# Optimization experiments

Hardware: AMD Instinct MI355X
Metric: run time of the kernel (lower is better)

The kernel has to match this reference:

```python
import jax, jax.numpy as jnp
import numpy as np

NUM_FEATS = 65536
IN_SIZE = 1024
OUT_SIZE = 1024
NUM_MODULES = 8


def setup_inputs() -> dict:
    key = jax.random.key(0)
    k1, k2, k3, k4 = jax.random.split(key, 4)
    in_feats = jax.random.normal(k1, (NUM_FEATS, IN_SIZE), dtype=jnp.float32)
    module_ids = jax.random.randint(k2, (NUM_FEATS,), 0, NUM_MODULES, dtype=jnp.int64)
    # Per-expert Linear parameters (same architecture, different weights).
    # PyTorch nn.Linear default init: U(-1/sqrt(in), 1/sqrt(in)).
    bound = 1.0 / np.sqrt(IN_SIZE)
    W = jax.random.uniform(k3, (NUM_MODULES, IN_SIZE, OUT_SIZE), jnp.float32, -bound, bound)
    b = jax.random.uniform(k4, (NUM_MODULES, OUT_SIZE), jnp.float32, -bound, bound)
    return {"in_feats": in_feats, "module_ids": module_ids, "W": W, "b": b}


def reference(in_feats, module_ids, W, b):
    # Faithful to: out[mask_e] = Linear_e(in_feats[mask_e]) for each expert e.
    # Vectorized as a fixed small loop over experts with masked combine
    # (no Python loop over the data dimension).
    num_feats = in_feats.shape[0]
    out = jnp.zeros((num_feats, OUT_SIZE), dtype=in_feats.dtype)
    for e in range(NUM_MODULES):
        y = in_feats @ W[e] + b[e]  # [num_feats, OUT_SIZE]
        mask = (module_ids == e)[:, None]
        out = jnp.where(mask, y, out)
    return out
```

## Files before the change

kernel.cpp:

```cpp
#include <hip/hip_runtime.h>

typedef unsigned short u16;
typedef unsigned int u32;
typedef __attribute__((ext_vector_type(8))) short short8;
typedef __attribute__((ext_vector_type(4))) float f32x4;

#define NF 65536
#define KDIM 1024
#define NDIM 1024
#define NE 8
#define BM 128
#define BN 128
#define MAX_MT (NF / BM + NE)
#define GEMM_GRID (MAX_MT * 8)
#define TILE_B 16384
#define SORT_BLOCKS 64

#define AS1 __attribute__((address_space(1)))
#define AS3 __attribute__((address_space(3)))

__device__ __forceinline__ u16 f2bf(float f) {
  u32 u = __float_as_uint(f);
  u += 0x7FFF + ((u >> 16) & 1);
  return (u16)(u >> 16);
}

__device__ __forceinline__ int swz8(int r) {
  return (r & 7) ^ ((r >> 3) & 7);
}
__device__ __forceinline__ int swz_slot(int r) { return swz8(r) << 4; }

__device__ __forceinline__ void cp16(void* l, const void* g) {
  __builtin_amdgcn_global_load_lds((const AS1 unsigned int*)g,
                                   (AS3 unsigned int*)l, 16, 0, 0);
}

__global__ void k_cnt(const int* __restrict__ ids, int* __restrict__ gcnt) {
  __shared__ int wc[16][NE];
  int b = blockIdx.x, t = threadIdx.x;
  int w = t >> 6, lane = t & 63;
  if (t < 16 * NE) ((int*)wc)[t] = 0;
  __syncthreads();
  for (int s = 0; s < 4; ++s) {
    int i = (b << 10) + (s << 8) + t;
    int e = ids[i];
#pragma unroll
    for (int ee = 0; ee < NE; ++ee) {
      unsigned long long mask = __ballot(e == ee);
      if (lane == 0) wc[(s << 2) + w][ee] = (int)__popcll(mask);
    }
  }
  __syncthreads();
  if (t < NE) {
    int sum = 0;
#pragma unroll
    for (int j = 0; j < 16; ++j) sum += wc[j][t];
    gcnt[b * NE + t] = sum;
  }
}

__global__ void k_excl(const int* __restrict__ gcnt, int* __restrict__ counts,
                       int* __restrict__ offsets, int* __restrict__ tile_base,
                       int* __restrict__ base) {
  __shared__ int tot[NE], offs[NE];
  int t = threadIdx.x;
  if (t < NE) {
    int s = 0;
    for (int b = 0; b < SORT_BLOCKS; ++b) s += gcnt[b * NE + t];
    tot[t] = s;
    counts[t] = s;
  }
  __syncthreads();
  if (t == 0) {
    int run = 0, tb = 0;
    tile_base[0] = 0;
    for (int e = 0; e < NE; ++e) {
      offsets[e] = run;
      offs[e] = run;
      run += tot[e];
      tb += (tot[e] + BM - 1) / BM;
      tile_base[e + 1] = tb;
    }
  }
  __syncthreads();
  if (t < NE) {
    int run = offs[t];
    for (int b = 0; b < SORT_BLOCKS; ++b) {
      base[b * NE + t] = run;
      run += gcnt[b * NE + t];
    }
  }
}

__global__ void k_place(const int* __restrict__ ids, const int* __restrict__ base,
                        int* __restrict__ perm) {
  __shared__ int wc[16][NE], wsc[16][NE];
  int b = blockIdx.x, t = threadIdx.x;
  int w = t >> 6, lane = t & 63;
  for (int s = 0; s < 4; ++s) {
    int i = (b << 10) + (s << 8) + t;
    int e = ids[i];
#pragma unroll
    for (int ee = 0; ee < NE; ++ee) {
      unsigned long long mask = __ballot(e == ee);
      if (lane == 0) wc[(s << 2) + w][ee] = (int)__popcll(mask);
    }
  }
  __syncthreads();
  if (t < NE) {
    int run = 0;
#pragma unroll
    for (int j = 0; j < 16; ++j) {
      wsc[j][t] = run;
      run += wc[j][t];
    }
  }
  __syncthreads();
  for (int s = 0; s < 4; ++s) {
    int i = (b << 10) + (s << 8) + t;
    int e = ids[i];
#pragma unroll
    for (int ee = 0; ee < NE; ++ee) {
      unsigned long long mask = __ballot(e == ee);
      if (e == ee) {
        int rank = (int)__popcll(mask & ((1ull << lane) - 1ull));
        perm[base[b * NE + e] + wsc[(s << 2) + w][e] + rank] = i;
      }
    }
  }
}

__global__ void k_aconv(const float* __restrict__ A, const int* __restrict__ perm,
                        const int* __restrict__ counts,
                        const int* __restrict__ offsets,
                        const int* __restrict__ tile_base, u16* __restrict__ Abf) {
  int b = blockIdx.x;
  int mt = b >> 4, kt = b & 15;
  if (mt >= tile_base[NE]) return;
  int e = 0;
#pragma unroll
  for (int ee = 0; ee < NE - 1; ++ee)
    if (mt >= tile_base[ee + 1]) e = ee + 1;
  int mloc = mt - tile_base[e];
  int row_base = offsets[e] + (mloc << 7);
  int rim = counts[e] - (mloc << 7);
  rim = rim < BM ? rim : BM;
  int tid = threadIdx.x;
  char* dst = (char*)Abf + (size_t)b * TILE_B;
#pragma unroll
  for (int i = 0; i < 4; ++i) {
    int o = (i << 12) + (tid << 4);
    int r = o >> 7;
    int s = ((o >> 4) & 7) ^ swz8(r);
    uint4 pkt = make_uint4(0, 0, 0, 0);
    if (r < rim) {
      int g = perm[row_base + r];
      const float* src = A + (size_t)g * KDIM + (kt << 6) + (s << 3);
      float4 v0 = ((const float4*)src)[0];
      float4 v1 = ((const float4*)src)[1];
      pkt.x = (u32)f2bf(v0.x) | ((u32)f2bf(v0.y) << 16);
      pkt.y = (u32)f2bf(v0.z) | ((u32)f2bf(v0.w) << 16);
      pkt.z = (u32)f2bf(v1.x) | ((u32)f2bf(v1.y) << 16);
      pkt.w = (u32)f2bf(v1.z) | ((u32)f2bf(v1.w) << 16);
    }
    *(uint4*)(dst + o) = pkt;
  }
}

__global__ void k_wconv2(const float* __restrict__ W, u16* __restrict__ Wt) {
  int b = blockIdx.x;
  int e = b >> 7, nt = (b >> 4) & 7, kt = b & 15;
  int tid = threadIdx.x;
  const float* We = W + ((size_t)e << 20);
  char* dst = (char*)Wt + (size_t)b * TILE_B;
#pragma unroll
  for (int i = 0; i < 4; ++i) {
    int o = (i << 12) + (tid << 4);
    int r = o >> 7;
    int s = ((o >> 4) & 7) ^ swz8(r);
    int n = (nt << 7) + r;
    int k = (kt << 6) + (s << 3);
    u32 p[4];
#pragma unroll
    for (int j = 0; j < 4; ++j) {
      u32 lo = f2bf(We[(size_t)(k + 2 * j) * NDIM + n]);
      u32 hi = f2bf(We[(size_t)(k + 2 * j + 1) * NDIM + n]);
      p[j] = lo | (hi << 16);
    }
    *(uint4*)(dst + o) = make_uint4(p[0], p[1], p[2], p[3]);
  }
}

__global__ __launch_bounds__(256, 4) void k_gemm_fast(
    const u16* __restrict__ Abf, const u16* __restrict__ Wt,
    const float* __restrict__ bias, const int* __restrict__ perm,
    const int* __restrict__ offsets, const int* __restrict__ counts,
    const int* __restrict__ tile_base, float* __restrict__ out) {
  int bid = blockIdx.x;
  const int cpx = GEMM_GRID >> 3;
  int l = (bid & 7) * cpx + (bid >> 3);
  int mt = l >> 3, nt = l & 7;
  if (mt >= tile_base[NE]) return;
  int e = 0;
#pragma unroll
  for (int ee = 0; ee < NE - 1; ++ee)
    if (mt >= tile_base[ee + 1]) e = ee + 1;
  int mloc = mt - tile_base[e];
  int row_base = offsets[e] + (mloc << 7);
  int rim = counts[e] - (mloc << 7);
  rim = rim < BM ? rim : BM;
  int n0 = nt << 7;

  __shared__ __align__(16) char lds[2 * TILE_B];
  char* la = lds;
  char* lb = lds + TILE_B;

  int tid = threadIdx.x;
  int lane = tid & 63, wid = tid >> 6;
  int wr = wid >> 1, wc = wid & 1;
  int l15 = lane & 15;
  int lk2 = (lane >> 4) << 4;

  const char* srcA = (const char*)Abf + (size_t)(mt << 4) * TILE_B;
  const char* srcB = (const char*)Wt + (size_t)(((e << 3) + nt) << 4) * TILE_B;

  int ar_addr[4], br_addr[4];
#pragma unroll
  for (int m = 0; m < 4; ++m) {
    int r = (wr << 6) + (m << 4) + l15;
    ar_addr[m] = r * 128 + (lk2 ^ swz_slot(r));
  }
#pragma unroll
  for (int n = 0; n < 4; ++n) {
    int r = (wc << 6) + (n << 4) + l15;
    br_addr[n] = r * 128 + (lk2 ^ swz_slot(r));
  }

  f32x4 acc[4][4];
#pragma unroll
  for (int m = 0; m < 4; ++m)
#pragma unroll
    for (int n = 0; n < 4; ++n) acc[m][n] = f32x4{0.f, 0.f, 0.f, 0.f};

  int toff = tid << 4;
#pragma unroll 1
  for (int kt = 0; kt < KDIM / 64; ++kt) {
    __syncthreads();
    const char* ga = srcA + kt * TILE_B;
    const char* gb = srcB + kt * TILE_B;
#pragma unroll
    for (int j = 0; j < 4; ++j) cp16(la + toff + (j << 12), ga + toff + (j << 12));
#pragma unroll
    for (int j = 0; j < 4; ++j) cp16(lb + toff + (j << 12), gb + toff + (j << 12));
    asm volatile("s_waitcnt vmcnt(0)" ::: "memory");
    __builtin_amdgcn_sched_barrier(0);
    __syncthreads();
#pragma unroll
    for (int kk = 0; kk < 2; ++kk) {
      int kx = kk << 6;
      short8 af[4], bfr[4];
#pragma unroll
      for (int m = 0; m < 4; ++m)
        af[m] = __builtin_bit_cast(short8, *(const uint4*)(la + (ar_addr[m] ^ kx)));
#pragma unroll
      for (int n = 0; n < 4; ++n)
        bfr[n] = __builtin_bit_cast(short8, *(const uint4*)(lb + (br_addr[n] ^ kx)));
#pragma unroll
      for (int m = 0; m < 4; ++m)
#pragma unroll
        for (int n = 0; n < 4; ++n)
          acc[m][n] = __builtin_amdgcn_mfma_f32_16x16x32_bf16(af[m], bfr[n],
                                                              acc[m][n], 0, 0, 0);
    }
  }

  float bv[4];
#pragma unroll
  for (int n = 0; n < 4; ++n)
    bv[n] = bias[(e << 10) + n0 + (wc << 6) + (n << 4) + l15];
  int rq = (lane >> 4) << 2;
#pragma unroll
  for (int m = 0; m < 4; ++m) {
#pragma unroll
    for (int j = 0; j < 4; ++j) {
      int rl = (wr << 6) + (m << 4) + rq + j;
      if (rl < rim) {
        int grow = perm[row_base + rl];
        float* orow = out + (size_t)grow * NDIM + n0 + (wc << 6) + l15;
#pragma unroll
        for (int n = 0; n < 4; ++n) orow[n << 4] = acc[m][n][j] + bv[n];
      }
    }
  }
}

__global__ __launch_bounds__(256, 3) void k_gemm_slow(
    const float* __restrict__ A, const float* __restrict__ W,
    const float* __restrict__ bias, const int* __restrict__ perm,
    const int* __restrict__ offsets, const int* __restrict__ counts,
    const int* __restrict__ tile_base, float* __restrict__ out) {
  int bid = blockIdx.x;
  const int cpx = GEMM_GRID >> 3;
  int l = (bid & 7) * cpx + (bid >> 3);
  int mt = l >> 3, nt = l & 7;
  if (mt >= tile_base[NE]) return;
  int e = 0;
#pragma unroll
  for (int ee = 0; ee < NE - 1; ++ee)
    if (mt >= tile_base[ee + 1]) e = ee + 1;
  int mloc = mt - tile_base[e];
  int row_base = offsets[e] + (mloc << 7);
  int rim = counts[e] - (mloc << 7);
  rim = rim < BM ? rim : BM;
  int n0 = nt << 7;

  __shared__ u16 Al[BM * 64];
  __shared__ u16 Bl[BN * 64];
  char* alb = (char*)Al;
  char* blb = (char*)Bl;

  int tid = threadIdx.x;
  int lane = tid & 63, wid = tid >> 6;
  int wr = wid >> 1, wc = wid & 1;
  int l15 = lane & 15;
  int lk2 = (lane >> 4) << 4;

  int acol4 = tid & 15, argp = tid >> 4;
  const float* arow_p[8];
  int aswz[8];
#pragma unroll
  for (int i = 0; i < 8; ++i) {
    int r = argp + (i << 4);
    int rr = r < rim ? r : rim - 1;
    int grow = perm[row_base + rr];
    arow_p[i] = A + (size_t)grow * KDIM + (acol4 << 2);
    aswz[i] = r * 128 + ((acol4 << 3) ^ swz_slot(r));
  }
  int bnloc = tid & 127;
  int bkh = tid >> 7;
  const float* bcol_f = W + ((size_t)e << 20) + n0 + bnloc;
  int bswz[4];
#pragma unroll
  for (int j = 0; j < 4; ++j)
    bswz[j] = bnloc * 128 + (((bkh << 6) + (j << 4)) ^ swz_slot(bnloc));

  int ar_addr[4], br_addr[4];
#pragma unroll
  for (int m = 0; m < 4; ++m) {
    int r = (wr << 6) + (m << 4) + l15;
    ar_addr[m] = r * 128 + (lk2 ^ swz_slot(r));
  }
#pragma unroll
  for (int n = 0; n < 4; ++n) {
    int r = (wc << 6) + (n << 4) + l15;
    br_addr[n] = r * 128 + (lk2 ^ swz_slot(r));
  }

  f32x4 acc[4][4];
#pragma unroll
  for (int m = 0; m < 4; ++m)
#pragma unroll
    for (int n = 0; n < 4; ++n) acc[m][n] = f32x4{0.f, 0.f, 0.f, 0.f};

#pragma unroll 1
  for (int kt = 0; kt < KDIM / 64; ++kt) {
    int k0 = kt << 6;
    __syncthreads();
#pragma unroll
    for (int i = 0; i < 8; ++i) {
      float4 v = *(const float4*)(arow_p[i] + k0);
      u32 lo = (u32)f2bf(v.x) | ((u32)f2bf(v.y) << 16);
      u32 hi = (u32)f2bf(v.z) | ((u32)f2bf(v.w) << 16);
      *(uint2*)(alb + aswz[i]) = make_uint2(lo, hi);
    }
    float vv[32];
#pragma unroll
    for (int i = 0; i < 32; ++i)
      vv[i] = bcol_f[(size_t)(k0 + (bkh << 5) + i) << 10];
#pragma unroll
    for (int j = 0; j < 4; ++j) {
      uint4 pkt;
      pkt.x = (u32)f2bf(vv[j * 8 + 0]) | ((u32)f2bf(vv[j * 8 + 1]) << 16);
      pkt.y = (u32)f2bf(vv[j * 8 + 2]) | ((u32)f2bf(vv[j * 8 + 3]) << 16);
      pkt.z = (u32)f2bf(vv[j * 8 + 4]) | ((u32)f2bf(vv[j * 8 + 5]) << 16);
      pkt.w = (u32)f2bf(vv[j * 8 + 6]) | ((u32)f2bf(vv[j * 8 + 7]) << 16);
      *(uint4*)(blb + bswz[j]) = pkt;
    }
    __syncthreads();
#pragma unroll
    for (int kk = 0; kk < 2; ++kk) {
      int kx = kk << 6;
      short8 af[4], bfr[4];
#pragma unroll
      for (int m = 0; m < 4; ++m)
        af[m] = __builtin_bit_cast(short8, *(const uint4*)(alb + (ar_addr[m] ^ kx)));
#pragma unroll
      for (int n = 0; n < 4; ++n)
        bfr[n] = __builtin_bit_cast(short8, *(const uint4*)(blb + (br_addr[n] ^ kx)));
#pragma unroll
      for (int m = 0; m < 4; ++m)
#pragma unroll
        for (int n = 0; n < 4; ++n)
          acc[m][n] = __builtin_amdgcn_mfma_f32_16x16x32_bf16(af[m], bfr[n],
                                                              acc[m][n], 0, 0, 0);
    }
  }

  float bv[4];
#pragma unroll
  for (int n = 0; n < 4; ++n)
    bv[n] = bias[(e << 10) + n0 + (wc << 6) + (n << 4) + l15];
  int rq = (lane >> 4) << 2;
#pragma unroll
  for (int m = 0; m < 4; ++m) {
#pragma unroll
    for (int j = 0; j < 4; ++j) {
      int rl = (wr << 6) + (m << 4) + rq + j;
      if (rl < rim) {
        int grow = perm[row_base + rl];
        float* orow = out + (size_t)grow * NDIM + n0 + (wc << 6) + l15;
#pragma unroll
        for (int n = 0; n < 4; ++n) orow[n << 4] = acc[m][n][j] + bv[n];
      }
    }
  }
}

extern "C" void kernel_launch(void* const* d_in, const int* in_sizes, int n_in,
                              void* d_out, int out_size, void* d_ws,
                              size_t ws_size, hipStream_t stream) {
  const float* A = (const float*)d_in[0];
  const int* ids = (const int*)d_in[1];
  const float* W = (const float*)d_in[2];
  const float* bias = (const float*)d_in[3];
  float* out = (float*)d_out;

  char* ws = (char*)d_ws;
  int* counts = (int*)ws;
  int* offsets = (int*)(ws + 32);
  int* tile_base = (int*)(ws + 64);
  int* gcnt = (int*)(ws + 128);
  int* base = (int*)(ws + 2176);
  int* perm = (int*)(ws + 8192);
  const size_t abf_off = 524288;
  const size_t abf_sz = (size_t)MAX_MT * 16 * TILE_B;
  const size_t wt_off = abf_off + abf_sz;
  const size_t wt_sz = (size_t)NE * 8 * 16 * TILE_B;
  u16* Abf = (u16*)(ws + abf_off);
  u16* Wt = (u16*)(ws + wt_off);
  bool fast = ws_size >= wt_off + wt_sz;

  k_cnt<<<SORT_BLOCKS, 256, 0, stream>>>(ids, gcnt);
  k_excl<<<1, 64, 0, stream>>>(gcnt, counts, offsets, tile_base, base);
  k_place<<<SORT_BLOCKS, 256, 0, stream>>>(ids, base, perm);
  if (fast) {
    k_wconv2<<<NE * 8 * 16, 256, 0, stream>>>(W, Wt);
    k_aconv<<<MAX_MT * 16, 256, 0, stream>>>(A, perm, counts, offsets,
                                             tile_base, Abf);
    k_gemm_fast<<<GEMM_GRID, 256, 0, stream>>>(Abf, Wt, bias, perm, offsets,
                                               counts, tile_base, out);
  } else {
    k_gemm_slow<<<GEMM_GRID, 256, 0, stream>>>(A, W, bias, perm, offsets,
                                               counts, tile_base, out);
  }
}
```

Baseline: 306.9 us.

## Fuse activation gather and bf16 conversion into the grouped GEMM

Removes the separate kernel that gathered permuted rows of A and converted them to swizzled bf16 tiles. The GEMM now gathers fp32 rows of A straight into LDS via per-row global_load_lds and converts to bf16 while building MFMA fragments. This avoids writing and re-reading an intermediate bf16 copy of A. In exchange, each N-tile re-reads fp32 A, doubling A bytes per GEMM pass and LDS per block, and occupancy is lowered to 3 blocks.

```diff
diff --git a/kernel.cpp b/kernel.cpp
--- a/kernel.cpp
+++ b/kernel.cpp
@@ -29,6 +29,9 @@
   return (r & 7) ^ ((r >> 3) & 7);
 }
 __device__ __forceinline__ int swz_slot(int r) { return swz8(r) << 4; }
+__device__ __forceinline__ int amsk(int r) {
+  return (swz8(r) << 1) | (r & 1);
+}
 
 __device__ __forceinline__ void cp16(void* l, const void* g) {
   __builtin_amdgcn_global_load_lds((const AS1 unsigned int*)g,
@@ -130,43 +133,6 @@
   }
 }
 
-__global__ void k_aconv(const float* __restrict__ A, const int* __restrict__ perm,
-                        const int* __restrict__ counts,
-                        const int* __restrict__ offsets,
-                        const int* __restrict__ tile_base, u16* __restrict__ Abf) {
-  int b = blockIdx.x;
-  int mt = b >> 4, kt = b & 15;
-  if (mt >= tile_base[NE]) return;
-  int e = 0;
-#pragma unroll
-  for (int ee = 0; ee < NE - 1; ++ee)
-    if (mt >= tile_base[ee + 1]) e = ee + 1;
-  int mloc = mt - tile_base[e];
-  int row_base = offsets[e] + (mloc << 7);
-  int rim = counts[e] - (mloc << 7);
-  rim = rim < BM ? rim : BM;
-  int tid = threadIdx.x;
-  char* dst = (char*)Abf + (size_t)b * TILE_B;
-#pragma unroll
-  for (int i = 0; i < 4; ++i) {
-    int o = (i << 12) + (tid << 4);
-    int r = o >> 7;
-    int s = ((o >> 4) & 7) ^ swz8(r);
-    uint4 pkt = make_uint4(0, 0, 0, 0);
-    if (r < rim) {
-      int g = perm[row_base + r];
-      const float* src = A + (size_t)g * KDIM + (kt << 6) + (s << 3);
-      float4 v0 = ((const float4*)src)[0];
-      float4 v1 = ((const float4*)src)[1];
-      pkt.x = (u32)f2bf(v0.x) | ((u32)f2bf(v0.y) << 16);
-      pkt.y = (u32)f2bf(v0.z) | ((u32)f2bf(v0.w) << 16);
-      pkt.z = (u32)f2bf(v1.x) | ((u32)f2bf(v1.y) << 16);
-      pkt.w = (u32)f2bf(v1.z) | ((u32)f2bf(v1.w) << 16);
-    }
-    *(uint4*)(dst + o) = pkt;
-  }
-}
-
 __global__ void k_wconv2(const float* __restrict__ W, u16* __restrict__ Wt) {
   int b = blockIdx.x;
   int e = b >> 7, nt = (b >> 4) & 7, kt = b & 15;
@@ -191,8 +157,8 @@
   }
 }
 
-__global__ __launch_bounds__(256, 4) void k_gemm_fast(
-    const u16* __restrict__ Abf, const u16* __restrict__ Wt,
+__global__ __launch_bounds__(256, 3) void k_gemm_fused(
+    const float* __restrict__ A, const u16* __restrict__ Wt,
     const float* __restrict__ bias, const int* __restrict__ perm,
     const int* __restrict__ offsets, const int* __restrict__ counts,
     const int* __restrict__ tile_base, float* __restrict__ out) {
@@ -211,29 +177,42 @@
   rim = rim < BM ? rim : BM;
   int n0 = nt << 7;
 
-  __shared__ __align__(16) char lds[2 * TILE_B];
-  char* la = lds;
-  char* lb = lds + TILE_B;
+  __shared__ __align__(16) char ldsA[BM * 64 * 4];
+  __shared__ __align__(16) char ldsB[BN * 64 * 2];
 
   int tid = threadIdx.x;
   int lane = tid & 63, wid = tid >> 6;
   int wr = wid >> 1, wc = wid & 1;
   int l15 = lane & 15;
-  int lk2 = (lane >> 4) << 4;
-
-  const char* srcA = (const char*)Abf + (size_t)(mt << 4) * TILE_B;
+  int q4 = lane >> 4;
+  int lk2 = q4 << 4;
+
+  u32 aoff[8];
+#pragma unroll
+  for (int j = 0; j < 8; ++j) {
+    int r = (wid << 5) + (j << 2) + q4;
+    int rr = r < rim ? r : rim - 1;
+    int g = perm[row_base + rr];
+    int t = l15 ^ amsk(r);
+    aoff[j] = ((u32)g << 12) + ((u32)t << 4);
+  }
+  int adst = (wid << 13) + (lane << 4);
+  const char* Ab = (const char*)A;
+
   const char* srcB = (const char*)Wt + (size_t)(((e << 3) + nt) << 4) * TILE_B;
-
-  int ar_addr[4], br_addr[4];
+  int toff = tid << 4;
+
+  int ar_addr[4];
 #pragma unroll
   for (int m = 0; m < 4; ++m) {
     int r = (wr << 6) + (m << 4) + l15;
-    ar_addr[m] = r * 128 + (lk2 ^ swz_slot(r));
-  }
+    ar_addr[m] = (r << 8) + (((q4 << 1) ^ amsk(r)) << 4);
+  }
+  int br_addr[4];
 #pragma unroll
   for (int n = 0; n < 4; ++n) {
     int r = (wc << 6) + (n << 4) + l15;
-    br_addr[n] = r * 128 + (lk2 ^ swz_slot(r));
+    br_addr[n] = (r << 7) + (lk2 ^ swz_slot(r));
   }
 
   f32x4 acc[4][4];
@@ -242,29 +221,37 @@
 #pragma unroll
     for (int n = 0; n < 4; ++n) acc[m][n] = f32x4{0.f, 0.f, 0.f, 0.f};
 
-  int toff = tid << 4;
 #pragma unroll 1
   for (int kt = 0; kt < KDIM / 64; ++kt) {
     __syncthreads();
-    const char* ga = srcA + kt * TILE_B;
-    const char* gb = srcB + kt * TILE_B;
-#pragma unroll
-    for (int j = 0; j < 4; ++j) cp16(la + toff + (j << 12), ga + toff + (j << 12));
-#pragma unroll
-    for (int j = 0; j < 4; ++j) cp16(lb + toff + (j << 12), gb + toff + (j << 12));
+    u32 kb = (u32)kt << 8;
+#pragma unroll
+    for (int j = 0; j < 8; ++j)
+      cp16(ldsA + adst + (j << 10), Ab + (aoff[j] + kb));
+    const char* gb = srcB + ((size_t)kt << 14);
+#pragma unroll
+    for (int j = 0; j < 4; ++j) cp16(ldsB + toff + (j << 12), gb + toff + (j << 12));
     asm volatile("s_waitcnt vmcnt(0)" ::: "memory");
     __builtin_amdgcn_sched_barrier(0);
     __syncthreads();
 #pragma unroll
     for (int kk = 0; kk < 2; ++kk) {
-      int kx = kk << 6;
       short8 af[4], bfr[4];
 #pragma unroll
-      for (int m = 0; m < 4; ++m)
-        af[m] = __builtin_bit_cast(short8, *(const uint4*)(la + (ar_addr[m] ^ kx)));
+      for (int m = 0; m < 4; ++m) {
+        int a0 = ar_addr[m] ^ (kk << 7);
+        f32x4 lo = *(const f32x4*)(ldsA + a0);
+        f32x4 hi = *(const f32x4*)(ldsA + (a0 ^ 16));
+        u32 p0 = (u32)f2bf(lo[0]) | ((u32)f2bf(lo[1]) << 16);
+        u32 p1 = (u32)f2bf(lo[2]) | ((u32)f2bf(lo[3]) << 16);
+        u32 p2 = (u32)f2bf(hi[0]) | ((u32)f2bf(hi[1]) << 16);
+        u32 p3 = (u32)f2bf(hi[2]) | ((u32)f2bf(hi[3]) << 16);
+        af[m] = __builtin_bit_cast(short8, make_uint4(p0, p1, p2, p3));
+      }
 #pragma unroll
       for (int n = 0; n < 4; ++n)
-        bfr[n] = __builtin_bit_cast(short8, *(const uint4*)(lb + (br_addr[n] ^ kx)));
+        bfr[n] = __builtin_bit_cast(short8,
+                                    *(const uint4*)(ldsB + (br_addr[n] ^ (kk << 6))));
 #pragma unroll
       for (int m = 0; m < 4; ++m)
 #pragma unroll
@@ -442,11 +429,8 @@
   int* gcnt = (int*)(ws + 128);
   int* base = (int*)(ws + 2176);
   int* perm = (int*)(ws + 8192);
-  const size_t abf_off = 524288;
-  const size_t abf_sz = (size_t)MAX_MT * 16 * TILE_B;
-  const size_t wt_off = abf_off + abf_sz;
+  const size_t wt_off = 524288;
   const size_t wt_sz = (size_t)NE * 8 * 16 * TILE_B;
-  u16* Abf = (u16*)(ws + abf_off);
   u16* Wt = (u16*)(ws + wt_off);
   bool fast = ws_size >= wt_off + wt_sz;
 
@@ -455,10 +439,8 @@
   k_place<<<SORT_BLOCKS, 256, 0, stream>>>(ids, base, perm);
   if (fast) {
     k_wconv2<<<NE * 8 * 16, 256, 0, stream>>>(W, Wt);
-    k_aconv<<<MAX_MT * 16, 256, 0, stream>>>(A, perm, counts, offsets,
-                                             tile_base, Abf);
-    k_gemm_fast<<<GEMM_GRID, 256, 0, stream>>>(Abf, Wt, bias, perm, offsets,
-                                               counts, tile_base, out);
+    k_gemm_fused<<<GEMM_GRID, 256, 0, stream>>>(A, Wt, bias, perm, offsets,
+                                                counts, tile_base, out);
   } else {
     k_gemm_slow<<<GEMM_GRID, 256, 0, stream>>>(A, W, bias, perm, offsets,
                                                counts, tile_base, out);
```

After: 320.0 us. +4.3%, slower.

## Replace grouped GEMM with 256x256-tile, 8-wave, multi-stage LDS pipelined kernel

Applied to the files above, without the earlier changes.

The fast-path GEMM now uses 256x256 output tiles with 512 threads (8 waves) and a 5-slot, 160KB dynamic LDS ring. Global-to-LDS copies for the next k-steps are issued in interleaved phases between MFMA groups, and setprio raises wave priority around the math. Expert segments are padded to multiples of 256 rows, so k_excl emits a new super-tile prefix array and k_aconv lays out A to match. Bf16 packing in the A conversion now uses the hardware v_cvt_pk_bf16_f32 instruction. The intent is to cut per-iteration sync stalls and raise data reuse per tile, at the cost of more padding waste per expert, one block per CU from the LDS footprint, and heavy register pressure from 32 accumulators.

```diff
diff --git a/kernel.cpp b/kernel.cpp
--- a/kernel.cpp
+++ b/kernel.cpp
@@ -10,29 +10,40 @@
 #define NDIM 1024
 #define NE 8
 #define BM 128
-#define BN 128
 #define MAX_MT (NF / BM + NE)
 #define GEMM_GRID (MAX_MT * 8)
 #define TILE_B 16384
 #define SORT_BLOCKS 64
+#define MAX_ST 264
+#define GRID8 (MAX_ST * 4)
+#define LDSZ (5 * 32768)
 
 #define AS1 __attribute__((address_space(1)))
 #define AS3 __attribute__((address_space(3)))
+
+#define BAR __builtin_amdgcn_s_barrier()
+#define WAITV4                                        \
+  asm volatile("s_waitcnt vmcnt(4)" ::: "memory");    \
+  __builtin_amdgcn_sched_barrier(0)
+#define WAITL0                                        \
+  asm volatile("s_waitcnt lgkmcnt(0)" ::: "memory");  \
+  __builtin_amdgcn_sched_barrier(0)
 
 __device__ __forceinline__ u16 f2bf(float f) {
   u32 u = __float_as_uint(f);
   u += 0x7FFF + ((u >> 16) & 1);
   return (u16)(u >> 16);
 }
-
-__device__ __forceinline__ int swz8(int r) {
-  return (r & 7) ^ ((r >> 3) & 7);
-}
+__device__ __forceinline__ int swz8(int r) { return (r & 7) ^ ((r >> 3) & 7); }
 __device__ __forceinline__ int swz_slot(int r) { return swz8(r) << 4; }
-
 __device__ __forceinline__ void cp16(void* l, const void* g) {
   __builtin_amdgcn_global_load_lds((const AS1 unsigned int*)g,
                                    (AS3 unsigned int*)l, 16, 0, 0);
+}
+__device__ __forceinline__ u32 cvtpk(float a, float b) {
+  u32 r;
+  asm("v_cvt_pk_bf16_f32 %0, %1, %2" : "=v"(r) : "v"(a), "v"(b));
+  return r;
 }
 
 __global__ void k_cnt(const int* __restrict__ ids, int* __restrict__ gcnt) {
@@ -61,7 +72,7 @@
 
 __global__ void k_excl(const int* __restrict__ gcnt, int* __restrict__ counts,
                        int* __restrict__ offsets, int* __restrict__ tile_base,
-                       int* __restrict__ base) {
+                       int* __restrict__ stb, int* __restrict__ base) {
   __shared__ int tot[NE], offs[NE];
   int t = threadIdx.x;
   if (t < NE) {
@@ -72,14 +83,17 @@
   }
   __syncthreads();
   if (t == 0) {
-    int run = 0, tb = 0;
+    int run = 0, tb = 0, sb = 0;
     tile_base[0] = 0;
+    stb[0] = 0;
     for (int e = 0; e < NE; ++e) {
       offsets[e] = run;
       offs[e] = run;
       run += tot[e];
       tb += (tot[e] + BM - 1) / BM;
       tile_base[e + 1] = tb;
+      sb += (tot[e] + 255) / 256;
+      stb[e + 1] = sb;
     }
   }
   __syncthreads();
@@ -133,20 +147,20 @@
 __global__ void k_aconv(const float* __restrict__ A, const int* __restrict__ perm,
                         const int* __restrict__ counts,
                         const int* __restrict__ offsets,
-                        const int* __restrict__ tile_base, u16* __restrict__ Abf) {
+                        const int* __restrict__ stb, u16* __restrict__ Abf) {
   int b = blockIdx.x;
-  int mt = b >> 4, kt = b & 15;
-  if (mt >= tile_base[NE]) return;
+  int a = b >> 4, kt = b & 15;
+  if (a >= (stb[NE] << 1)) return;
   int e = 0;
 #pragma unroll
   for (int ee = 0; ee < NE - 1; ++ee)
-    if (mt >= tile_base[ee + 1]) e = ee + 1;
-  int mloc = mt - tile_base[e];
-  int row_base = offsets[e] + (mloc << 7);
-  int rim = counts[e] - (mloc << 7);
+    if (a >= (stb[ee + 1] << 1)) e = ee + 1;
+  int loc = a - (stb[e] << 1);
+  int row_base = offsets[e] + (loc << 7);
+  int rim = counts[e] - (loc << 7);
   rim = rim < BM ? rim : BM;
   int tid = threadIdx.x;
-  char* dst = (char*)Abf + (size_t)b * TILE_B;
+  char* dst = (char*)Abf + (size_t)(a * 16 + kt) * TILE_B;
 #pragma unroll
   for (int i = 0; i < 4; ++i) {
     int o = (i << 12) + (tid << 4);
@@ -158,10 +172,10 @@
       const float* src = A + (size_t)g * KDIM + (kt << 6) + (s << 3);
       float4 v0 = ((const float4*)src)[0];
       float4 v1 = ((const float4*)src)[1];
-      pkt.x = (u32)f2bf(v0.x) | ((u32)f2bf(v0.y) << 16);
-      pkt.y = (u32)f2bf(v0.z) | ((u32)f2bf(v0.w) << 16);
-      pkt.z = (u32)f2bf(v1.x) | ((u32)f2bf(v1.y) << 16);
-      pkt.w = (u32)f2bf(v1.z) | ((u32)f2bf(v1.w) << 16);
+      pkt.x = cvtpk(v0.x, v0.y);
+      pkt.y = cvtpk(v0.z, v0.w);
+      pkt.z = cvtpk(v1.x, v1.y);
+      pkt.w = cvtpk(v1.z, v1.w);
     }
     *(uint4*)(dst + o) = pkt;
   }
@@ -191,102 +205,192 @@
   }
 }
 
-__global__ __launch_bounds__(256, 4) void k_gemm_fast(
+__global__ __launch_bounds__(512, 2) void k_gemm_8p(
     const u16* __restrict__ Abf, const u16* __restrict__ Wt,
     const float* __restrict__ bias, const int* __restrict__ perm,
     const int* __restrict__ offsets, const int* __restrict__ counts,
-    const int* __restrict__ tile_base, float* __restrict__ out) {
+    const int* __restrict__ stb, float* __restrict__ out) {
+  extern __shared__ __align__(16) char lds[];
   int bid = blockIdx.x;
-  const int cpx = GEMM_GRID >> 3;
-  int l = (bid & 7) * cpx + (bid >> 3);
-  int mt = l >> 3, nt = l & 7;
-  if (mt >= tile_base[NE]) return;
+  int l = (bid & 7) * (GRID8 >> 3) + (bid >> 3);
+  int st = l >> 2, nt2 = l & 3;
+  if (st >= stb[NE]) return;
   int e = 0;
 #pragma unroll
   for (int ee = 0; ee < NE - 1; ++ee)
-    if (mt >= tile_base[ee + 1]) e = ee + 1;
-  int mloc = mt - tile_base[e];
-  int row_base = offsets[e] + (mloc << 7);
-  int rim = counts[e] - (mloc << 7);
-  rim = rim < BM ? rim : BM;
-  int n0 = nt << 7;
-
-  __shared__ __align__(16) char lds[2 * TILE_B];
-  char* la = lds;
-  char* lb = lds + TILE_B;
+    if (st >= stb[ee + 1]) e = ee + 1;
+  int sloc = st - stb[e];
+  int row_base = offsets[e] + (sloc << 8);
+  int rim = counts[e] - (sloc << 8);
+  rim = rim < 256 ? rim : 256;
 
   int tid = threadIdx.x;
   int lane = tid & 63, wid = tid >> 6;
-  int wr = wid >> 1, wc = wid & 1;
-  int l15 = lane & 15;
-  int lk2 = (lane >> 4) << 4;
-
-  const char* srcA = (const char*)Abf + (size_t)(mt << 4) * TILE_B;
-  const char* srcB = (const char*)Wt + (size_t)(((e << 3) + nt) << 4) * TILE_B;
-
-  int ar_addr[4], br_addr[4];
-#pragma unroll
-  for (int m = 0; m < 4; ++m) {
-    int r = (wr << 6) + (m << 4) + l15;
-    ar_addr[m] = r * 128 + (lk2 ^ swz_slot(r));
+  int wr = wid >> 2, wc = wid & 3, w2 = wc >> 1;
+  int l15 = lane & 15, q4 = lane >> 4, lk2 = q4 << 4;
+  int t16 = tid << 4;
+
+  const char* Ab0 = (const char*)Abf + (size_t)((st << 1) + 0) * 16 * TILE_B;
+  const char* Ab1 = (const char*)Abf + (size_t)((st << 1) + 1) * 16 * TILE_B;
+  const char* Bb0 =
+      (const char*)Wt + (size_t)(((e << 3) + (nt2 << 1) + 0) * 16) * TILE_B;
+  const char* Bb1 =
+      (const char*)Wt + (size_t)(((e << 3) + (nt2 << 1) + 1) * 16) * TILE_B;
+
+  int arx[8], brx[4];
+#pragma unroll
+  for (int m = 0; m < 8; ++m) {
+    int r = (m << 4) + l15;
+    arx[m] = (r << 7) + (lk2 ^ swz_slot(r));
   }
 #pragma unroll
   for (int n = 0; n < 4; ++n) {
-    int r = (wc << 6) + (n << 4) + l15;
-    br_addr[n] = r * 128 + (lk2 ^ swz_slot(r));
-  }
-
-  f32x4 acc[4][4];
-#pragma unroll
-  for (int m = 0; m < 4; ++m)
+    int r = ((wc & 1) << 6) + (n << 4) + l15;
+    brx[n] = (r << 7) + (lk2 ^ swz_slot(r));
+  }
+
+  f32x4 acc[8][4];
+#pragma unroll
+  for (int m = 0; m < 8; ++m)
 #pragma unroll
     for (int n = 0; n < 4; ++n) acc[m][n] = f32x4{0.f, 0.f, 0.f, 0.f};
 
-  int toff = tid << 4;
+  {
+    const char* sa[3] = {Ab0, Ab1, Ab0 + TILE_B};
+    const char* sb[3] = {Bb0, Bb1, Bb0 + TILE_B};
+#pragma unroll
+    for (int h = 0; h < 3; ++h) {
+      char* d = lds + (h << 15);
+#pragma unroll
+      for (int j = 0; j < 2; ++j) {
+        cp16(d + (j << 13) + t16, sa[h] + (j << 13) + t16);
+        cp16(d + 16384 + (j << 13) + t16, sb[h] + (j << 13) + t16);
+      }
+    }
+  }
+  WAITV4;
+  BAR;
+
+  int s0 = 0;
 #pragma unroll 1
-  for (int kt = 0; kt < KDIM / 64; ++kt) {
-    __syncthreads();
-    const char* ga = srcA + kt * TILE_B;
-    const char* gb = srcB + kt * TILE_B;
-#pragma unroll
-    for (int j = 0; j < 4; ++j) cp16(la + toff + (j << 12), ga + toff + (j << 12));
-#pragma unroll
-    for (int j = 0; j < 4; ++j) cp16(lb + toff + (j << 12), gb + toff + (j << 12));
-    asm volatile("s_waitcnt vmcnt(0)" ::: "memory");
-    __builtin_amdgcn_sched_barrier(0);
-    __syncthreads();
-#pragma unroll
-    for (int kk = 0; kk < 2; ++kk) {
-      int kx = kk << 6;
-      short8 af[4], bfr[4];
-#pragma unroll
-      for (int m = 0; m < 4; ++m)
-        af[m] = __builtin_bit_cast(short8, *(const uint4*)(la + (ar_addr[m] ^ kx)));
+  for (int t = 0; t < 16; ++t) {
+    int sA = s0 + wr;
+    sA = sA >= 5 ? sA - 5 : sA;
+    int sB = s0 + w2;
+    sB = sB >= 5 ? sB - 5 : sB;
+    const char* pa = lds + (sA << 15);
+    const char* pb = lds + (sB << 15) + 16384;
+    int sx = s0 + 3;
+    sx = sx >= 5 ? sx - 5 : sx;
+    int sy = s0 + 4;
+    sy = sy >= 5 ? sy - 5 : sy;
+    char* dx = lds + (sx << 15);
+    char* dy = lds + (sy << 15);
+    size_t o1 = (size_t)(t + 1 < 16 ? t + 1 : 15) * TILE_B;
+    size_t o2 = (size_t)(t + 2 < 16 ? t + 2 : 15) * TILE_B;
+    const char* gA1 = Ab1 + o1;
+    const char* gB1 = Bb1 + o1;
+    const char* gA0 = Ab0 + o2;
+    const char* gB0 = Bb0 + o2;
+    short8 bfr[4];
+    {
+      short8 afr[4];
+#pragma unroll
+      for (int n = 0; n < 4; ++n) bfr[n] = *(const short8*)(pb + brx[n]);
+#pragma unroll
+      for (int i = 0; i < 4; ++i) afr[i] = *(const short8*)(pa + arx[i]);
+      cp16(dx + t16, gA1 + t16);
+      cp16(dx + 16384 + t16, gB1 + t16);
+      BAR;
+      WAITL0;
+      __builtin_amdgcn_s_setprio(1);
+#pragma unroll
+      for (int i = 0; i < 4; ++i)
+#pragma unroll
+        for (int n = 0; n < 4; ++n)
+          acc[i][n] = __builtin_amdgcn_mfma_f32_16x16x32_bf16(afr[i], bfr[n],
+                                                              acc[i][n], 0, 0, 0);
+      __builtin_amdgcn_s_setprio(0);
+      BAR;
+    }
+    {
+      short8 afr[4];
+#pragma unroll
+      for (int i = 0; i < 4; ++i) afr[i] = *(const short8*)(pa + arx[4 + i]);
+      cp16(dx + 8192 + t16, gA1 + 8192 + t16);
+      cp16(dx + 16384 + 8192 + t16, gB1 + 8192 + t16);
+      BAR;
+      WAITL0;
+      __builtin_amdgcn_s_setprio(1);
+#pragma unroll
+      for (int i = 0; i < 4; ++i)
+#pragma unroll
+        for (int n = 0; n < 4; ++n)
+          acc[4 + i][n] = __builtin_amdgcn_mfma_f32_16x16x32_bf16(
+              afr[i], bfr[n], acc[4 + i][n], 0, 0, 0);
+      __builtin_amdgcn_s_setprio(0);
+      BAR;
+    }
+    {
+      short8 afr[4];
 #pragma unroll
       for (int n = 0; n < 4; ++n)
-        bfr[n] = __builtin_bit_cast(short8, *(const uint4*)(lb + (br_addr[n] ^ kx)));
-#pragma unroll
-      for (int m = 0; m < 4; ++m)
+        bfr[n] = *(const short8*)(pb + (brx[n] ^ 64));
+#pragma unroll
+      for (int i = 0; i < 4; ++i)
+        afr[i] = *(const short8*)(pa + (arx[i] ^ 64));
+      cp16(dy + t16, gA0 + t16);
+      cp16(dy + 16384 + t16, gB0 + t16);
+      BAR;
+      WAITL0;
+      __builtin_amdgcn_s_setprio(1);
+#pragma unroll
+      for (int i = 0; i < 4; ++i)
 #pragma unroll
         for (int n = 0; n < 4; ++n)
-          acc[m][n] = __builtin_amdgcn_mfma_f32_16x16x32_bf16(af[m], bfr[n],
-                                                              acc[m][n], 0, 0, 0);
-    }
+          acc[i][n] = __builtin_amdgcn_mfma_f32_16x16x32_bf16(afr[i], bfr[n],
+                                                              acc[i][n], 0, 0, 0);
+      __builtin_amdgcn_s_setprio(0);
+      BAR;
+    }
+    {
+      short8 afr[4];
+#pragma unroll
+      for (int i = 0; i < 4; ++i)
+        afr[i] = *(const short8*)(pa + (arx[4 + i] ^ 64));
+      cp16(dy + 8192 + t16, gA0 + 8192 + t16);
+      cp16(dy + 16384 + 8192 + t16, gB0 + 8192 + t16);
+      BAR;
+      WAITL0;
+      __builtin_amdgcn_s_setprio(1);
+#pragma unroll
+      for (int i = 0; i < 4; ++i)
+#pragma unroll
+        for (int n = 0; n < 4; ++n)
+          acc[4 + i][n] = __builtin_amdgcn_mfma_f32_16x16x32_bf16(
+              afr[i], bfr[n], acc[4 + i][n], 0, 0, 0);
+      __builtin_amdgcn_s_setprio(0);
+      WAITV4;
+      BAR;
+    }
+    s0 += 2;
+    s0 = s0 >= 5 ? s0 - 5 : s0;
   }
 
   float bv[4];
 #pragma unroll
   for (int n = 0; n < 4; ++n)
-    bv[n] = bias[(e << 10) + n0 + (wc << 6) + (n << 4) + l15];
-  int rq = (lane >> 4) << 2;
-#pragma unroll
-  for (int m = 0; m < 4; ++m) {
+    bv[n] = bias[(e << 10) + (nt2 << 8) + (wc << 6) + (n << 4) + l15];
+  int rq = q4 << 2;
+#pragma unroll
+  for (int m = 0; m < 8; ++m) {
 #pragma unroll
     for (int j = 0; j < 4; ++j) {
-      int rl = (wr << 6) + (m << 4) + rq + j;
+      int rl = (wr << 7) + (m << 4) + rq + j;
       if (rl < rim) {
         int grow = perm[row_base + rl];
-        float* orow = out + (size_t)grow * NDIM + n0 + (wc << 6) + l15;
+        float* orow =
+            out + (size_t)grow * NDIM + (nt2 << 8) + (wc << 6) + l15;
 #pragma unroll
         for (int n = 0; n < 4; ++n) orow[n << 4] = acc[m][n][j] + bv[n];
       }
@@ -315,13 +419,13 @@
   int n0 = nt << 7;
 
   __shared__ u16 Al[BM * 64];
-  __shared__ u16 Bl[BN * 64];
+  __shared__ u16 Bl[BM * 64];
   char* alb = (char*)Al;
   char* blb = (char*)Bl;
 
   int tid = threadIdx.x;
   int lane = tid & 63, wid = tid >> 6;
-  int wr = wid >> 1, wc = wid & 1;
+  int wr = wid >> 1, wcc = wid & 1;
   int l15 = lane & 15;
   int lk2 = (lane >> 4) << 4;
 
@@ -352,7 +456,7 @@
   }
 #pragma unroll
   for (int n = 0; n < 4; ++n) {
-    int r = (wc << 6) + (n << 4) + l15;
+    int r = (wcc << 6) + (n << 4) + l15;
     br_addr[n] = r * 128 + (lk2 ^ swz_slot(r));
   }
 
@@ -409,7 +513,7 @@
   float bv[4];
 #pragma unroll
   for (int n = 0; n < 4; ++n)
-    bv[n] = bias[(e << 10) + n0 + (wc << 6) + (n << 4) + l15];
+    bv[n] = bias[(e << 10) + n0 + (wcc << 6) + (n << 4) + l15];
   int rq = (lane >> 4) << 2;
 #pragma unroll
   for (int m = 0; m < 4; ++m) {
@@ -418,7 +522,7 @@
       int rl = (wr << 6) + (m << 4) + rq + j;
       if (rl < rim) {
         int grow = perm[row_base + rl];
-        float* orow = out + (size_t)grow * NDIM + n0 + (wc << 6) + l15;
+        float* orow = out + (size_t)grow * NDIM + n0 + (wcc << 6) + l15;
 #pragma unroll
         for (int n = 0; n < 4; ++n) orow[n << 4] = acc[m][n][j] + bv[n];
       }
@@ -439,26 +543,33 @@
   int* counts = (int*)ws;
   int* offsets = (int*)(ws + 32);
   int* tile_base = (int*)(ws + 64);
-  int* gcnt = (int*)(ws + 128);
-  int* base = (int*)(ws + 2176);
+  int* stb = (int*)(ws + 112);
+  int* gcnt = (int*)(ws + 160);
+  int* base = (int*)(ws + 2208);
   int* perm = (int*)(ws + 8192);
   const size_t abf_off = 524288;
-  const size_t abf_sz = (size_t)MAX_MT * 16 * TILE_B;
+  const size_t abf_sz = (size_t)2 * MAX_ST * 16 * TILE_B;
   const size_t wt_off = abf_off + abf_sz;
   const size_t wt_sz = (size_t)NE * 8 * 16 * TILE_B;
   u16* Abf = (u16*)(ws + abf_off);
   u16* Wt = (u16*)(ws + wt_off);
   bool fast = ws_size >= wt_off + wt_sz;
+  if (fast) {
+    hipError_t err = hipFuncSetAttribute(
+        (const void*)k_gemm_8p, hipFuncAttributeMaxDynamicSharedMemorySize,
+        LDSZ);
+    if (err != hipSuccess) fast = false;
+  }
 
   k_cnt<<<SORT_BLOCKS, 256, 0, stream>>>(ids, gcnt);
-  k_excl<<<1, 64, 0, stream>>>(gcnt, counts, offsets, tile_base, base);
+  k_excl<<<1, 64, 0, stream>>>(gcnt, counts, offsets, tile_base, stb, base);
   k_place<<<SORT_BLOCKS, 256, 0, stream>>>(ids, base, perm);
   if (fast) {
     k_wconv2<<<NE * 8 * 16, 256, 0, stream>>>(W, Wt);
-    k_aconv<<<MAX_MT * 16, 256, 0, stream>>>(A, perm, counts, offsets,
-                                             tile_base, Abf);
-    k_gemm_fast<<<GEMM_GRID, 256, 0, stream>>>(Abf, Wt, bias, perm, offsets,
-                                               counts, tile_base, out);
+    k_aconv<<<2 * MAX_ST * 16, 256, 0, stream>>>(A, perm, counts, offsets, stb,
+                                                 Abf);
+    k_gemm_8p<<<GRID8, 512, LDSZ, stream>>>(Abf, Wt, bias, perm, offsets,
+                                            counts, stb, out);
   } else {
     k_gemm_slow<<<GEMM_GRID, 256, 0, stream>>>(A, W, bias, perm, offsets,
                                                counts, tile_base, out);
```

Result: slower. 331.1 us (+7.9%).
